# Performance work log

Hardware: AMD Instinct MI355X
Metric: run time of the kernel (lower is better)

## Reference

```python
import jax, jax.numpy as jnp
import numpy as np

N = 100000   # nodes
E = 1600000  # edges
IN, HID, CLS = 128, 64, 32


def gcn_conv(x, src, dst, W, b, num_nodes):
    """PyG-style GCNConv: out = D^{-1/2} (A+I) D^{-1/2} X W + b."""
    xw = x @ W  # transform first (matches PyG: propagate on transformed feats)
    loop = jnp.arange(num_nodes)
    src_f = jnp.concatenate([src, loop])
    dst_f = jnp.concatenate([dst, loop])
    ones = jnp.ones(src_f.shape[0], dtype=xw.dtype)
    deg = jax.ops.segment_sum(ones, dst_f, num_segments=num_nodes)
    dinv = jnp.where(deg > 0, jax.lax.rsqrt(deg), 0.0)
    norm = dinv[src_f] * dinv[dst_f]            # [E+N]
    msg = xw[src_f] * norm[:, None]             # gather + scale
    out = jax.ops.segment_sum(msg, dst_f, num_segments=num_nodes)
    return out + b


def setup_inputs() -> dict:
    key = jax.random.key(0)
    k = jax.random.split(key, 7)
    x = jax.random.normal(k[0], (N, IN), dtype=jnp.float32)
    edge_index = jax.random.randint(k[1], (2, E), 0, N)
    edge_attr = jax.random.normal(k[2], (E, 1), dtype=jnp.float32)
    W1 = jax.random.normal(k[3], (IN, HID), dtype=jnp.float32) / np.sqrt(IN)
    b1 = jnp.zeros((HID,), dtype=jnp.float32)
    W2 = jax.random.normal(k[4], (HID, CLS), dtype=jnp.float32) / np.sqrt(HID)
    b2 = jnp.zeros((CLS,), dtype=jnp.float32)
    return {"x": x, "edge_index": edge_index, "edge_attr": edge_attr,
            "W1": W1, "b1": b1, "W2": W2, "b2": b2}


def reference(x, edge_index, edge_attr, W1, b1, W2, b2):
    # edge_attr is unpacked by the original forward but unused by GCNConv
    src, dst = edge_index[0], edge_index[1]
    h = jax.nn.relu(gcn_conv(x, src, dst, W1, b1, N))
    return gcn_conv(h, src, dst, W2, b2, N)
```

## Files before the change

kernel.cpp:

```cpp
#include <hip/hip_runtime.h>
#include <hip/hip_fp16.h>

#define N_NODES 100000
#define N_EDGES 1600000
#define IN_F 128
#define HID_F 64
#define CLS_F 32

#define NBKT 512
#define BKT_NODES 196
#define EPB 16384
#define NBLK 98
#define NVAL (NBKT * NBLK)
#define CAPB 5120

typedef short s8v __attribute__((ext_vector_type(8)));
typedef float f4v __attribute__((ext_vector_type(4)));

__device__ __forceinline__ unsigned short f2b(float f) {
    union { float f; unsigned i; } c; c.f = f;
    unsigned r = c.i + 0x7FFFu + ((c.i >> 16) & 1u);
    return (unsigned short)(r >> 16);
}
__device__ __forceinline__ unsigned short f2h(float f) {
    return __half_as_ushort(__float2half_rn(f));
}


__global__ __launch_bounds__(256) void bucketA_kernel(const int* __restrict__ dst,
                                                      int* __restrict__ bh) {
    __shared__ int h[NBKT];
    for (int i = threadIdx.x; i < NBKT; i += 256) h[i] = 0;
    __syncthreads();
    int e0 = blockIdx.x * EPB;
    int e1 = min(e0 + EPB, N_EDGES);
    for (int e = e0 + threadIdx.x; e < e1; e += 256)
        atomicAdd(&h[dst[e] / BKT_NODES], 1);
    __syncthreads();
    for (int i = threadIdx.x; i < NBKT; i += 256)
        bh[i * NBLK + blockIdx.x] = h[i];
}

__global__ __launch_bounds__(1024) void scan_hist_kernel(int* __restrict__ bh) {
    __shared__ int wsum[16];
    const int CH = (NVAL + 1023) / 1024;
    int t = threadIdx.x;
    int base = t * CH;
    int v[CH];
    int local = 0;
#pragma unroll
    for (int i = 0; i < CH; i++) {
        int idx = base + i;
        int x = (idx < NVAL) ? bh[idx] : 0;
        v[i] = local;
        local += x;
    }
    int lane = t & 63, w = t >> 6;
    int s = local;
#pragma unroll
    for (int d = 1; d < 64; d <<= 1) {
        int u = __shfl_up(s, d);
        if (lane >= d) s += u;
    }
    if (lane == 63) wsum[w] = s;
    __syncthreads();
    int wbase = 0;
    for (int i = 0; i < w; i++) wbase += wsum[i];
    int tbase = wbase + s - local;
#pragma unroll
    for (int i = 0; i < CH; i++) {
        int idx = base + i;
        if (idx < NVAL) bh[idx] = tbase + v[i];
    }
}

__global__ __launch_bounds__(256) void bucketB_kernel(const int* __restrict__ src,
                                                      const int* __restrict__ dst,
                                                      const int* __restrict__ bhScan,
                                                      unsigned* __restrict__ bkt) {
    __shared__ int cur[NBKT];
    for (int i = threadIdx.x; i < NBKT; i += 256)
        cur[i] = bhScan[i * NBLK + blockIdx.x];
    __syncthreads();
    int e0 = blockIdx.x * EPB;
    int e1 = min(e0 + EPB, N_EDGES);
    for (int e = e0 + threadIdx.x; e < e1; e += 256) {
        int d = dst[e];
        int g = d / BKT_NODES;
        unsigned pk = ((unsigned)(d - g * BKT_NODES) << 17) | (unsigned)src[e];
        int pos = atomicAdd(&cur[g], 1);
        bkt[pos] = pk;
    }
}

__global__ __launch_bounds__(256) void sort_bucket_kernel(const int* __restrict__ bhScan,
                                                          const unsigned* __restrict__ bkt,
                                                          int* __restrict__ csr,
                                                          int* __restrict__ off,
                                                          int* __restrict__ endp,
                                                          float* __restrict__ dinv) {
    __shared__ int hist[BKT_NODES];
    __shared__ int loff[BKT_NODES];
    __shared__ int loffB[BKT_NODES];
    __shared__ int wt[4];
    __shared__ int csrS[CAPB];
    int b = blockIdx.x;
    int t = threadIdx.x;
    int s0 = bhScan[b * NBLK];
    int s1 = (b < NBKT - 1) ? bhScan[(b + 1) * NBLK] : N_EDGES;
    int nE = s1 - s0;

    for (int i = t; i < BKT_NODES; i += 256) hist[i] = 0;
    __syncthreads();
    for (int i = t; i < nE; i += 256)
        atomicAdd(&hist[bkt[s0 + i] >> 17], 1);
    __syncthreads();

    int h0 = 0, h1 = 0;
    if (t < 98) { h0 = hist[2 * t]; h1 = hist[2 * t + 1]; }
    int p0 = (h0 + 7) & ~7;
    int p1 = (h1 + 7) & ~7;
    int sum = p0 + p1;
    int lane = t & 63, w = t >> 6;
    int s = sum;
#pragma unroll
    for (int d = 1; d < 64; d <<= 1) {
        int u = __shfl_up(s, d);
        if (lane >= d) s += u;
    }
    if (lane == 63) wt[w] = s;
    __syncthreads();
    int wbase = 0;
    for (int i = 0; i < w; i++) wbase += wt[i];
    int excl = wbase + s - sum;
    if (t < 98) {
        loff[2 * t] = excl;         loffB[2 * t] = excl;
        loff[2 * t + 1] = excl + p0; loffB[2 * t + 1] = excl + p0;
    }
    __syncthreads();

    for (int j = t; j < BKT_NODES; j += 256) {
        int n = b * BKT_NODES + j;
        if (n < N_NODES) {
            int c = hist[j];
            int o = b * CAPB + loff[j];
            off[n] = o;
            endp[n] = o + ((c + 7) & ~7);
            dinv[n] = rsqrtf((float)(c + 1));
        }
    }
    __syncthreads();

    for (int i = t; i < nE; i += 256) {
        unsigned pk = bkt[s0 + i];
        int dl = (int)(pk >> 17);
        int p = atomicAdd(&loff[dl], 1);
        csrS[p] = (int)(pk & 0x1FFFFu);
    }
    __syncthreads();

    for (int j = t; j < BKT_NODES; j += 256) {
        int c = hist[j];
        int bse = loffB[j];
        int pe = bse + ((c + 7) & ~7);
        for (int p = bse + c; p < pe; p++) csrS[p] = N_NODES;
    }
    __syncthreads();

    int padTot = wt[0] + wt[1] + wt[2] + wt[3];
    for (int i = t; i < padTot; i += 256) csr[b * CAPB + i] = csrS[i];
}

#define XBM 64
__global__ __launch_bounds__(256) void xw1_kernel(const float* __restrict__ x,
                                                  const float* __restrict__ W1,
                                                  const float* __restrict__ dinv,
                                                  unsigned short* __restrict__ y1h) {
    __shared__ __align__(16) unsigned short Wb[16 * 64 * 8];
    __shared__ __align__(16) unsigned short xb[XBM][IN_F + 8];

    int tid = threadIdx.x;

    for (int i = tid; i < IN_F * HID_F; i += 256) {
        int k = i >> 6, n = i & 63;
        int kc = k >> 5, kw = k & 31;
        int nt = n >> 4, nl = n & 15;
        int quad = kw >> 3, j = kw & 7;
        Wb[(((kc * 4 + nt) * 64) + quad * 16 + nl) * 8 + j] = f2b(W1[i]);
    }

    int nodeBase = blockIdx.x * XBM;
    {
        int snl = tid >> 2;
        int sk0 = (tid & 3) * 32;
        int n = nodeBase + snl;
#pragma unroll
        for (int kk = 0; kk < 32; kk += 4) {
            float4 v = make_float4(0.f, 0.f, 0.f, 0.f);
            if (n < N_NODES) v = *(const float4*)(x + (size_t)n * IN_F + sk0 + kk);
            ushort4 o;
            o.x = f2b(v.x); o.y = f2b(v.y); o.z = f2b(v.z); o.w = f2b(v.w);
            *(ushort4*)(&xb[snl][sk0 + kk]) = o;
        }
    }
    __syncthreads();

    int wave = tid >> 6, lane = tid & 63;
    int quad = lane >> 4, l15 = lane & 15;
    int rowBase = wave * 16;

    f4v acc[4];
#pragma unroll
    for (int i = 0; i < 4; i++) acc[i] = (f4v){0.f, 0.f, 0.f, 0.f};

#pragma unroll
    for (int kc = 0; kc < 4; kc++) {
        s8v a = *(const s8v*)(&xb[rowBase + l15][kc * 32 + quad * 8]);
#pragma unroll
        for (int nt = 0; nt < 4; nt++) {
            s8v b = *(const s8v*)(&Wb[((kc * 4 + nt) * 64 + lane) * 8]);
            acc[nt] = __builtin_amdgcn_mfma_f32_16x16x32_bf16(a, b, acc[nt], 0, 0, 0);
        }
    }

    float dv[4];
    int n0 = nodeBase + rowBase + quad * 4;
#pragma unroll
    for (int r = 0; r < 4; r++)
        dv[r] = (n0 + r < N_NODES) ? dinv[n0 + r] : 0.f;
#pragma unroll
    for (int nt = 0; nt < 4; nt++) {
#pragma unroll
        for (int r = 0; r < 4; r++) {
            int n = n0 + r;
            if (n < N_NODES + 1)
                y1h[(size_t)n * HID_F + nt * 16 + l15] = f2h(acc[nt][r] * dv[r]);
        }
    }
}

__global__ __launch_bounds__(256) void gather1_fused_kernel(
        const int* __restrict__ off, const int* __restrict__ endp,
        const int* __restrict__ csr, const unsigned short* __restrict__ y1h,
        const float* __restrict__ dinv, const float* __restrict__ W2,
        const float* __restrict__ b1, unsigned short* __restrict__ y2h) {
    int tid = threadIdx.x;
    int wv = __builtin_amdgcn_readfirstlane(tid >> 6);
    int wave = blockIdx.x * 4 + wv;
    int nA = wave * 2;
    int lane = tid & 63;
    int half = lane >> 5;
    int cl = lane & 31;
    int k2 = 2 * cl;

    int offA = off[nA], offB = off[nA + 1];
    int lenA = endp[nA] - offA;
    int lenB = endp[nA + 1] - offB;
    const int* csA = csr + offA;
    const int* csB = csr + offB;
    const unsigned* y1u = (const unsigned*)y1h;

    int node = nA + half;
    unsigned su = y1u[(size_t)node * 32 + cl];
    union { unsigned u; __half2 h; } sc; sc.u = su;
    float sl = __half2float(sc.h.x), sh = __half2float(sc.h.y);
    float pa0 = half ? 0.f : sl, pa1 = half ? 0.f : sh;
    float pb0 = half ? sl : 0.f, pb1 = half ? sh : 0.f;

#define GP(P0, P1, SE, SO) { \
    int _i = half ? (SO) : (SE); \
    unsigned _u = y1u[(size_t)_i * 32 + cl]; \
    union { unsigned u; __half2 h; } _c; _c.u = _u; \
    P0 += __half2float(_c.h.x); P1 += __half2float(_c.h.y); }

    for (int tA = 0; tA < lenA; tA += 8) {
        int4 i0 = *(const int4*)(csA + tA);
        int4 i1 = *(const int4*)(csA + tA + 4);
        GP(pa0, pa1, i0.x, i0.y) GP(pa0, pa1, i0.z, i0.w)
        GP(pa0, pa1, i1.x, i1.y) GP(pa0, pa1, i1.z, i1.w)
    }
    for (int tB = 0; tB < lenB; tB += 8) {
        int4 i0 = *(const int4*)(csB + tB);
        int4 i1 = *(const int4*)(csB + tB + 4);
        GP(pb0, pb1, i0.x, i0.y) GP(pb0, pb1, i0.z, i0.w)
        GP(pb0, pb1, i1.x, i1.y) GP(pb0, pb1, i1.z, i1.w)
    }
#undef GP

    pa0 += __shfl_xor(pa0, 32); pa1 += __shfl_xor(pa1, 32);
    pb0 += __shfl_xor(pb0, 32); pb1 += __shfl_xor(pb1, 32);
    float a0 = half ? pb0 : pa0;
    float a1 = half ? pb1 : pa1;

    float dv = dinv[node];
    float2 bb = *(const float2*)(b1 + k2);
    float h0 = fmaxf(a0 * dv + bb.x, 0.f);
    float h1 = fmaxf(a1 * dv + bb.y, 0.f);

    float sum = 0.f;
#pragma unroll
    for (int t = 0; t < 32; t++) {
        float hh0 = __shfl(h0, t, 32);
        float hh1 = __shfl(h1, t, 32);
        sum += hh0 * W2[(2 * t) * CLS_F + cl] + hh1 * W2[(2 * t + 1) * CLS_F + cl];
    }
    y2h[(size_t)node * CLS_F + cl] = f2h(sum * dv);

    if (blockIdx.x == 0 && tid < 16)
        ((unsigned*)y2h)[(size_t)N_NODES * 16 + tid] = 0;
}

__global__ __launch_bounds__(256) void gather2_kernel(const int* __restrict__ off,
                                                      const int* __restrict__ endp,
                                                      const int* __restrict__ csr,
                                                      const unsigned short* __restrict__ y2h,
                                                      const float* __restrict__ dinv,
                                                      const float* __restrict__ b2,
                                                      float* __restrict__ out) {
    int tid = threadIdx.x;
    int wv = __builtin_amdgcn_readfirstlane(tid >> 6);
    int wave = blockIdx.x * 4 + wv;
    int n0 = wave * 4;
    int lane = tid & 63;
    int g = lane >> 4;
    int fl = lane & 15;
    int k2 = 2 * fl;
    const unsigned* y2u = (const unsigned*)y2h;

    int4 offs = *(const int4*)(off + n0);
    int4 ends = *(const int4*)(endp + n0);

    float r0 = 0.f, r1 = 0.f;

#define QS(P0, P1, IV) { \
    int _i = (g == 0) ? (IV).x : (g == 1) ? (IV).y : (g == 2) ? (IV).z : (IV).w; \
    unsigned _u = y2u[(size_t)_i * 16 + fl]; \
    union { unsigned u; __half2 h; } _c; _c.u = _u; \
    P0 += __half2float(_c.h.x); P1 += __half2float(_c.h.y); }

#pragma unroll
    for (int q = 0; q < 4; q++) {
        int o = (q == 0) ? offs.x : (q == 1) ? offs.y : (q == 2) ? offs.z : offs.w;
        int e = (q == 0) ? ends.x : (q == 1) ? ends.y : (q == 2) ? ends.z : ends.w;
        const int* cs = csr + o;
        int len = e - o;
        float p0 = 0.f, p1 = 0.f;
        for (int t = 0; t < len; t += 8) {
            int4 i0 = *(const int4*)(cs + t);
            int4 i1 = *(const int4*)(cs + t + 4);
            QS(p0, p1, i0) QS(p0, p1, i1)
        }
        p0 += __shfl_xor(p0, 32); p0 += __shfl_xor(p0, 16);
        p1 += __shfl_xor(p1, 32); p1 += __shfl_xor(p1, 16);
        if (g == q) { r0 = p0; r1 = p1; }
    }
#undef QS

    int node = n0 + g;
    unsigned su = y2u[(size_t)node * 16 + fl];
    union { unsigned u; __half2 h; } sc; sc.u = su;
    r0 += __half2float(sc.h.x);
    r1 += __half2float(sc.h.y);
    float dv = dinv[node];
    float2 bb = *(const float2*)(b2 + k2);
    float2 o2;
    o2.x = r0 * dv + bb.x;
    o2.y = r1 * dv + bb.y;
    *(float2*)(out + (size_t)node * CLS_F + k2) = o2;
}

extern "C" void kernel_launch(void* const* d_in, const int* in_sizes, int n_in,
                              void* d_out, int out_size, void* d_ws, size_t ws_size,
                              hipStream_t stream) {
    const float* x  = (const float*)d_in[0];
    const int*   ei = (const int*)d_in[1];
    const float* W1 = (const float*)d_in[3];
    const float* b1 = (const float*)d_in[4];
    const float* W2 = (const float*)d_in[5];
    const float* b2 = (const float*)d_in[6];
    float* out = (float*)d_out;

    const int* src = ei;
    const int* dst = ei + N_EDGES;

    char* ws = (char*)d_ws;
    size_t npad = ((size_t)N_NODES * 4 + 255) / 256 * 256;
    float* dinv = (float*)ws;
    int*   off  = (int*)(ws + npad);
    int*   endp = (int*)(ws + 2 * npad);
    int*   bh   = (int*)(ws + 3 * npad);
    int*   csr  = (int*)(ws + 3 * npad + 204800);
    char*  rbase = (char*)csr + (size_t)NBKT * CAPB * 4;
    unsigned* bkt = (unsigned*)rbase;
    unsigned short* y1h = (unsigned short*)rbase;
    unsigned short* y2h = (unsigned short*)(rbase + (size_t)(N_NODES + 1) * HID_F * 2);

    dim3 blk(256);
    bucketA_kernel  <<<dim3(NBLK), blk, 0, stream>>>(dst, bh);
    scan_hist_kernel<<<dim3(1), dim3(1024), 0, stream>>>(bh);
    bucketB_kernel  <<<dim3(NBLK), blk, 0, stream>>>(src, dst, bh, bkt);
    sort_bucket_kernel<<<dim3(NBKT), blk, 0, stream>>>(bh, bkt, csr, off, endp, dinv);
    xw1_kernel      <<<dim3((N_NODES + XBM - 1) / XBM), blk, 0, stream>>>(x, W1, dinv, y1h);
    gather1_fused_kernel<<<dim3(N_NODES / 8), blk, 0, stream>>>(off, endp, csr, y1h, dinv, W2, b1, y2h);
    gather2_kernel  <<<dim3(N_NODES / 16), blk, 0, stream>>>(off, endp, csr, y2h, dinv, b2, out);
}
```

Before: 259.7 us.

## Restructure gathers to 16-byte per-lane loads and split out MFMA second transform

The first gather now has each lane fetch 16 bytes (8 half features) from one neighbor, so a wave covers 8 neighbors per step with a software-prefetched index. The first-layer ReLU output is written to a new buffer, and a separate MFMA kernel then computes the second matmul instead of doing a shuffle-based matmul inside the gather. Gather2 is rewritten the same way with 8-byte loads and 2 nodes per wave. The first matmul switches from bf16 to fp16 MFMA. The aim is fewer, wider memory transactions and less shuffle-heavy ALU work, at the cost of one extra kernel launch and an extra write and read of the hidden features.

```diff
diff --git a/kernel.cpp b/kernel.cpp
--- a/kernel.cpp
+++ b/kernel.cpp
@@ -17,13 +17,30 @@
 typedef short s8v __attribute__((ext_vector_type(8)));
 typedef float f4v __attribute__((ext_vector_type(4)));
 
-__device__ __forceinline__ unsigned short f2b(float f) {
-    union { float f; unsigned i; } c; c.f = f;
-    unsigned r = c.i + 0x7FFFu + ((c.i >> 16) & 1u);
-    return (unsigned short)(r >> 16);
-}
 __device__ __forceinline__ unsigned short f2h(float f) {
     return __half_as_ushort(__float2half_rn(f));
+}
+__device__ __forceinline__ int packh2(float x, float y) {
+    __half2 p = __floats2half2_rn(x, y);
+    union { __half2 h; int i; } c; c.h = p; return c.i;
+}
+__device__ __forceinline__ void acc8(float* a, int4 v) {
+    union { int4 i; __half2 h[4]; } c; c.i = v;
+#pragma unroll
+    for (int j = 0; j < 4; j++) {
+        float2 f = __half22float2(c.h[j]);
+        a[2 * j] += f.x;
+        a[2 * j + 1] += f.y;
+    }
+}
+__device__ __forceinline__ void acc4(float* a, int2 v) {
+    union { int2 i; __half2 h[2]; } c; c.i = v;
+#pragma unroll
+    for (int j = 0; j < 2; j++) {
+        float2 f = __half22float2(c.h[j]);
+        a[2 * j] += f.x;
+        a[2 * j + 1] += f.y;
+    }
 }
 
 
@@ -186,7 +203,7 @@
         int kc = k >> 5, kw = k & 31;
         int nt = n >> 4, nl = n & 15;
         int quad = kw >> 3, j = kw & 7;
-        Wb[(((kc * 4 + nt) * 64) + quad * 16 + nl) * 8 + j] = f2b(W1[i]);
+        Wb[(((kc * 4 + nt) * 64) + quad * 16 + nl) * 8 + j] = f2h(W1[i]);
     }
 
     int nodeBase = blockIdx.x * XBM;
@@ -199,7 +216,7 @@
             float4 v = make_float4(0.f, 0.f, 0.f, 0.f);
             if (n < N_NODES) v = *(const float4*)(x + (size_t)n * IN_F + sk0 + kk);
             ushort4 o;
-            o.x = f2b(v.x); o.y = f2b(v.y); o.z = f2b(v.z); o.w = f2b(v.w);
+            o.x = f2h(v.x); o.y = f2h(v.y); o.z = f2h(v.z); o.w = f2h(v.w);
             *(ushort4*)(&xb[snl][sk0 + kk]) = o;
         }
     }
@@ -219,7 +236,7 @@
 #pragma unroll
         for (int nt = 0; nt < 4; nt++) {
             s8v b = *(const s8v*)(&Wb[((kc * 4 + nt) * 64 + lane) * 8]);
-            acc[nt] = __builtin_amdgcn_mfma_f32_16x16x32_bf16(a, b, acc[nt], 0, 0, 0);
+            acc[nt] = __builtin_amdgcn_mfma_f32_16x16x32_f16(a, b, acc[nt], 0, 0, 0);
         }
     }
 
@@ -239,75 +256,151 @@
     }
 }
 
-__global__ __launch_bounds__(256) void gather1_fused_kernel(
+__global__ __launch_bounds__(256) void gather1_kernel(
         const int* __restrict__ off, const int* __restrict__ endp,
         const int* __restrict__ csr, const unsigned short* __restrict__ y1h,
-        const float* __restrict__ dinv, const float* __restrict__ W2,
-        const float* __restrict__ b1, unsigned short* __restrict__ y2h) {
+        const float* __restrict__ dinv, const float* __restrict__ b1,
+        unsigned short* __restrict__ hout) {
     int tid = threadIdx.x;
     int wv = __builtin_amdgcn_readfirstlane(tid >> 6);
     int wave = blockIdx.x * 4 + wv;
-    int nA = wave * 2;
+    int nA = wave * 2, nB = nA + 1;
     int lane = tid & 63;
-    int half = lane >> 5;
-    int cl = lane & 31;
-    int k2 = 2 * cl;
-
-    int offA = off[nA], offB = off[nA + 1];
-    int lenA = endp[nA] - offA;
-    int lenB = endp[nA + 1] - offB;
-    const int* csA = csr + offA;
-    const int* csB = csr + offB;
-    const unsigned* y1u = (const unsigned*)y1h;
-
-    int node = nA + half;
-    unsigned su = y1u[(size_t)node * 32 + cl];
-    union { unsigned u; __half2 h; } sc; sc.u = su;
-    float sl = __half2float(sc.h.x), sh = __half2float(sc.h.y);
-    float pa0 = half ? 0.f : sl, pa1 = half ? 0.f : sh;
-    float pb0 = half ? sl : 0.f, pb1 = half ? sh : 0.f;
-
-#define GP(P0, P1, SE, SO) { \
-    int _i = half ? (SO) : (SE); \
-    unsigned _u = y1u[(size_t)_i * 32 + cl]; \
-    union { unsigned u; __half2 h; } _c; _c.u = _u; \
-    P0 += __half2float(_c.h.x); P1 += __half2float(_c.h.y); }
-
-    for (int tA = 0; tA < lenA; tA += 8) {
-        int4 i0 = *(const int4*)(csA + tA);
-        int4 i1 = *(const int4*)(csA + tA + 4);
-        GP(pa0, pa1, i0.x, i0.y) GP(pa0, pa1, i0.z, i0.w)
-        GP(pa0, pa1, i1.x, i1.y) GP(pa0, pa1, i1.z, i1.w)
-    }
-    for (int tB = 0; tB < lenB; tB += 8) {
-        int4 i0 = *(const int4*)(csB + tB);
-        int4 i1 = *(const int4*)(csB + tB + 4);
-        GP(pb0, pb1, i0.x, i0.y) GP(pb0, pb1, i0.z, i0.w)
-        GP(pb0, pb1, i1.x, i1.y) GP(pb0, pb1, i1.z, i1.w)
-    }
-#undef GP
-
-    pa0 += __shfl_xor(pa0, 32); pa1 += __shfl_xor(pa1, 32);
-    pb0 += __shfl_xor(pb0, 32); pb1 += __shfl_xor(pb1, 32);
-    float a0 = half ? pb0 : pa0;
-    float a1 = half ? pb1 : pa1;
-
-    float dv = dinv[node];
-    float2 bb = *(const float2*)(b1 + k2);
-    float h0 = fmaxf(a0 * dv + bb.x, 0.f);
-    float h1 = fmaxf(a1 * dv + bb.y, 0.f);
-
-    float sum = 0.f;
-#pragma unroll
-    for (int t = 0; t < 32; t++) {
-        float hh0 = __shfl(h0, t, 32);
-        float hh1 = __shfl(h1, t, 32);
-        sum += hh0 * W2[(2 * t) * CLS_F + cl] + hh1 * W2[(2 * t + 1) * CLS_F + cl];
-    }
-    y2h[(size_t)node * CLS_F + cl] = f2h(sum * dv);
-
-    if (blockIdx.x == 0 && tid < 16)
-        ((unsigned*)y2h)[(size_t)N_NODES * 16 + tid] = 0;
+    int f = lane & 7;
+    int g = lane >> 3;
+    int fo = f * 16;
+
+    int offA = off[nA], offB = off[nB];
+    int lenA = endp[nA] - offA, lenB = endp[nB] - offB;
+    const int* pA = csr + offA + g;
+    const int* pB = csr + offB + g;
+    const char* yb = (const char*)y1h;
+
+    float aA[8], aB[8];
+#pragma unroll
+    for (int j = 0; j < 8; j++) { aA[j] = 0.f; aB[j] = 0.f; }
+
+    int lmin = min(lenA, lenB);
+    int iA = pA[0], iB = pB[0];
+    int t = 0;
+    for (; t < lmin; t += 8) {
+        int icA = iA, icB = iB;
+        iA = pA[t + 8]; iB = pB[t + 8];
+        int4 vA = *(const int4*)(yb + (size_t)icA * 128 + fo);
+        int4 vB = *(const int4*)(yb + (size_t)icB * 128 + fo);
+        acc8(aA, vA); acc8(aB, vB);
+    }
+    for (; t < lenA; t += 8) {
+        int ic = iA; iA = pA[t + 8];
+        int4 v = *(const int4*)(yb + (size_t)ic * 128 + fo);
+        acc8(aA, v);
+    }
+    for (int u = lmin; u < lenB; u += 8) {
+        int ic = iB; iB = pB[u + 8];
+        int4 v = *(const int4*)(yb + (size_t)ic * 128 + fo);
+        acc8(aB, v);
+    }
+
+#pragma unroll
+    for (int m = 8; m <= 32; m <<= 1) {
+#pragma unroll
+        for (int j = 0; j < 8; j++) {
+            aA[j] += __shfl_xor(aA[j], m);
+            aB[j] += __shfl_xor(aB[j], m);
+        }
+    }
+
+    int4 sA = *(const int4*)(yb + (size_t)nA * 128 + fo);
+    int4 sB = *(const int4*)(yb + (size_t)nB * 128 + fo);
+    acc8(aA, sA); acc8(aB, sB);
+
+    float dvA = dinv[nA], dvB = dinv[nB];
+    float4 bl = *(const float4*)(b1 + 8 * f);
+    float4 bh4 = *(const float4*)(b1 + 8 * f + 4);
+    float bb[8] = {bl.x, bl.y, bl.z, bl.w, bh4.x, bh4.y, bh4.z, bh4.w};
+    float hA[8], hB[8];
+#pragma unroll
+    for (int j = 0; j < 8; j++) {
+        hA[j] = fmaxf(aA[j] * dvA + bb[j], 0.f);
+        hB[j] = fmaxf(aB[j] * dvB + bb[j], 0.f);
+    }
+    int4 HA, HB;
+    HA.x = packh2(hA[0], hA[1]); HA.y = packh2(hA[2], hA[3]);
+    HA.z = packh2(hA[4], hA[5]); HA.w = packh2(hA[6], hA[7]);
+    HB.x = packh2(hB[0], hB[1]); HB.y = packh2(hB[2], hB[3]);
+    HB.z = packh2(hB[4], hB[5]); HB.w = packh2(hB[6], hB[7]);
+
+    if (lane < 16) {
+        int node = (lane < 8) ? nA : nB;
+        int4 hv = (lane < 8) ? HA : HB;
+        *(int4*)((char*)hout + (size_t)node * 128 + (lane & 7) * 16) = hv;
+    }
+}
+
+#define YBM 64
+__global__ __launch_bounds__(256) void y2_kernel(const unsigned short* __restrict__ h,
+                                                 const float* __restrict__ W2,
+                                                 const float* __restrict__ dinv,
+                                                 unsigned short* __restrict__ y2h) {
+    __shared__ __align__(16) unsigned short Wb[2 * 2 * 64 * 8];
+    __shared__ __align__(16) unsigned short hb[YBM][HID_F + 8];
+    int tid = threadIdx.x;
+
+    for (int i = tid; i < HID_F * CLS_F; i += 256) {
+        int k = i >> 5, n = i & 31;
+        int kc = k >> 5, kw = k & 31;
+        int nt = n >> 4, nl = n & 15;
+        int quad = kw >> 3, j = kw & 7;
+        Wb[(((kc * 2 + nt) * 64) + quad * 16 + nl) * 8 + j] = f2h(W2[i]);
+    }
+
+    int nodeBase = blockIdx.x * YBM;
+    {
+        int row = tid >> 2, sseg = tid & 3;
+        int n = nodeBase + row;
+        int4 v0 = {0, 0, 0, 0}, v1 = {0, 0, 0, 0};
+        if (n < N_NODES) {
+            const char* hp = (const char*)h + (size_t)n * 128 + sseg * 32;
+            v0 = *(const int4*)hp;
+            v1 = *(const int4*)(hp + 16);
+        }
+        *(int4*)(&hb[row][sseg * 16]) = v0;
+        *(int4*)(&hb[row][sseg * 16 + 8]) = v1;
+    }
+    __syncthreads();
+
+    int wave = tid >> 6, lane = tid & 63;
+    int quad = lane >> 4, l15 = lane & 15;
+    int rowBase = wave * 16;
+
+    f4v acc[2];
+#pragma unroll
+    for (int i = 0; i < 2; i++) acc[i] = (f4v){0.f, 0.f, 0.f, 0.f};
+
+#pragma unroll
+    for (int kc = 0; kc < 2; kc++) {
+        s8v a = *(const s8v*)(&hb[rowBase + l15][kc * 32 + quad * 8]);
+#pragma unroll
+        for (int nt = 0; nt < 2; nt++) {
+            s8v b = *(const s8v*)(&Wb[((kc * 2 + nt) * 64 + lane) * 8]);
+            acc[nt] = __builtin_amdgcn_mfma_f32_16x16x32_f16(a, b, acc[nt], 0, 0, 0);
+        }
+    }
+
+    float dv[4];
+    int n0 = nodeBase + rowBase + quad * 4;
+#pragma unroll
+    for (int r = 0; r < 4; r++)
+        dv[r] = (n0 + r < N_NODES) ? dinv[n0 + r] : 0.f;
+#pragma unroll
+    for (int nt = 0; nt < 2; nt++) {
+#pragma unroll
+        for (int r = 0; r < 4; r++) {
+            int n = n0 + r;
+            if (n < N_NODES + 1)
+                y2h[(size_t)n * CLS_F + nt * 16 + l15] = f2h(acc[nt][r] * dv[r]);
+        }
+    }
 }
 
 __global__ __launch_bounds__(256) void gather2_kernel(const int* __restrict__ off,
@@ -320,53 +413,72 @@
     int tid = threadIdx.x;
     int wv = __builtin_amdgcn_readfirstlane(tid >> 6);
     int wave = blockIdx.x * 4 + wv;
-    int n0 = wave * 4;
+    int nA = wave * 2, nB = nA + 1;
     int lane = tid & 63;
-    int g = lane >> 4;
-    int fl = lane & 15;
-    int k2 = 2 * fl;
-    const unsigned* y2u = (const unsigned*)y2h;
-
-    int4 offs = *(const int4*)(off + n0);
-    int4 ends = *(const int4*)(endp + n0);
-
-    float r0 = 0.f, r1 = 0.f;
-
-#define QS(P0, P1, IV) { \
-    int _i = (g == 0) ? (IV).x : (g == 1) ? (IV).y : (g == 2) ? (IV).z : (IV).w; \
-    unsigned _u = y2u[(size_t)_i * 16 + fl]; \
-    union { unsigned u; __half2 h; } _c; _c.u = _u; \
-    P0 += __half2float(_c.h.x); P1 += __half2float(_c.h.y); }
-
-#pragma unroll
-    for (int q = 0; q < 4; q++) {
-        int o = (q == 0) ? offs.x : (q == 1) ? offs.y : (q == 2) ? offs.z : offs.w;
-        int e = (q == 0) ? ends.x : (q == 1) ? ends.y : (q == 2) ? ends.z : ends.w;
-        const int* cs = csr + o;
-        int len = e - o;
-        float p0 = 0.f, p1 = 0.f;
-        for (int t = 0; t < len; t += 8) {
-            int4 i0 = *(const int4*)(cs + t);
-            int4 i1 = *(const int4*)(cs + t + 4);
-            QS(p0, p1, i0) QS(p0, p1, i1)
-        }
-        p0 += __shfl_xor(p0, 32); p0 += __shfl_xor(p0, 16);
-        p1 += __shfl_xor(p1, 32); p1 += __shfl_xor(p1, 16);
-        if (g == q) { r0 = p0; r1 = p1; }
-    }
-#undef QS
-
-    int node = n0 + g;
-    unsigned su = y2u[(size_t)node * 16 + fl];
-    union { unsigned u; __half2 h; } sc; sc.u = su;
-    r0 += __half2float(sc.h.x);
-    r1 += __half2float(sc.h.y);
-    float dv = dinv[node];
-    float2 bb = *(const float2*)(b2 + k2);
-    float2 o2;
-    o2.x = r0 * dv + bb.x;
-    o2.y = r1 * dv + bb.y;
-    *(float2*)(out + (size_t)node * CLS_F + k2) = o2;
+    int f = lane & 7;
+    int g = lane >> 3;
+    int fo = f * 8;
+
+    int offA = off[nA], offB = off[nB];
+    int lenA = endp[nA] - offA, lenB = endp[nB] - offB;
+    const int* pA = csr + offA + g;
+    const int* pB = csr + offB + g;
+    const char* yb = (const char*)y2h;
+
+    float aA[4], aB[4];
+#pragma unroll
+    for (int j = 0; j < 4; j++) { aA[j] = 0.f; aB[j] = 0.f; }
+
+    int lmin = min(lenA, lenB);
+    int iA = pA[0], iB = pB[0];
+    int t = 0;
+    for (; t < lmin; t += 8) {
+        int icA = iA, icB = iB;
+        iA = pA[t + 8]; iB = pB[t + 8];
+        int2 vA = *(const int2*)(yb + (size_t)icA * 64 + fo);
+        int2 vB = *(const int2*)(yb + (size_t)icB * 64 + fo);
+        acc4(aA, vA); acc4(aB, vB);
+    }
+    for (; t < lenA; t += 8) {
+        int ic = iA; iA = pA[t + 8];
+        int2 v = *(const int2*)(yb + (size_t)ic * 64 + fo);
+        acc4(aA, v);
+    }
+    for (int u = lmin; u < lenB; u += 8) {
+        int ic = iB; iB = pB[u + 8];
+        int2 v = *(const int2*)(yb + (size_t)ic * 64 + fo);
+        acc4(aB, v);
+    }
+
+#pragma unroll
+    for (int m = 8; m <= 32; m <<= 1) {
+#pragma unroll
+        for (int j = 0; j < 4; j++) {
+            aA[j] += __shfl_xor(aA[j], m);
+            aB[j] += __shfl_xor(aB[j], m);
+        }
+    }
+
+    int2 sA = *(const int2*)(yb + (size_t)nA * 64 + fo);
+    int2 sB = *(const int2*)(yb + (size_t)nB * 64 + fo);
+    acc4(aA, sA); acc4(aB, sB);
+
+    float dvA = dinv[nA], dvB = dinv[nB];
+    float4 b2v = *(const float4*)(b2 + 4 * f);
+    float bbv[4] = {b2v.x, b2v.y, b2v.z, b2v.w};
+    float4 oA, oB;
+    float* oAp = (float*)&oA;
+    float* oBp = (float*)&oB;
+#pragma unroll
+    for (int j = 0; j < 4; j++) {
+        oAp[j] = aA[j] * dvA + bbv[j];
+        oBp[j] = aB[j] * dvB + bbv[j];
+    }
+    if (lane < 16) {
+        int node = (lane < 8) ? nA : nB;
+        float4 ov = (lane < 8) ? oA : oB;
+        *(float4*)(out + (size_t)node * CLS_F + (lane & 7) * 4) = ov;
+    }
 }
 
 extern "C" void kernel_launch(void* const* d_in, const int* in_sizes, int n_in,
@@ -394,6 +506,7 @@
     unsigned* bkt = (unsigned*)rbase;
     unsigned short* y1h = (unsigned short*)rbase;
     unsigned short* y2h = (unsigned short*)(rbase + (size_t)(N_NODES + 1) * HID_F * 2);
+    unsigned short* hbuf = (unsigned short*)((char*)y2h + (size_t)(N_NODES + 1) * CLS_F * 2);
 
     dim3 blk(256);
     bucketA_kernel  <<<dim3(NBLK), blk, 0, stream>>>(dst, bh);
@@ -401,6 +514,7 @@
     bucketB_kernel  <<<dim3(NBLK), blk, 0, stream>>>(src, dst, bh, bkt);
     sort_bucket_kernel<<<dim3(NBKT), blk, 0, stream>>>(bh, bkt, csr, off, endp, dinv);
     xw1_kernel      <<<dim3((N_NODES + XBM - 1) / XBM), blk, 0, stream>>>(x, W1, dinv, y1h);
-    gather1_fused_kernel<<<dim3(N_NODES / 8), blk, 0, stream>>>(off, endp, csr, y1h, dinv, W2, b1, y2h);
-    gather2_kernel  <<<dim3(N_NODES / 16), blk, 0, stream>>>(off, endp, csr, y2h, dinv, b2, out);
-}
+    gather1_kernel  <<<dim3(N_NODES / 8), blk, 0, stream>>>(off, endp, csr, y1h, dinv, b1, hbuf);
+    y2_kernel       <<<dim3((N_NODES + YBM) / YBM), blk, 0, stream>>>(hbuf, W2, dinv, y2h);
+    gather2_kernel  <<<dim3(N_NODES / 8), blk, 0, stream>>>(off, endp, csr, y2h, dinv, b2, out);
+}
```

Result: faster. 251.0 us (-3.4%).
